# Kernel optimization log

Hardware: AMD Instinct MI355X
Metric: run time of the kernel (lower is better)

Reference implementation:

```python
import jax, jax.numpy as jnp
import numpy as np

N_NODES = 50000
N_EDGES = 500000
F_DIM = 128
N_REL = 8
N_LAYERS = 2
NEG_SLOPE = 0.2  # PyG RGATConv default negative_slope


def setup_inputs() -> dict:
    key = jax.random.key(0)
    ks = jax.random.split(key, 6)
    x = jax.random.normal(ks[0], (N_NODES, F_DIM), dtype=jnp.float32)
    edge_index = jax.random.randint(ks[1], (2, N_EDGES), 0, N_NODES)
    edge_type = jax.random.randint(ks[2], (N_EDGES,), 0, N_REL)
    # Per-layer relation weights [L, R, F_in, F_out], attention vectors q,k [L, F_out, 1], bias [L, F_out]
    W = jax.random.normal(ks[3], (N_LAYERS, N_REL, F_DIM, F_DIM), dtype=jnp.float32) * (1.0 / np.sqrt(F_DIM)).astype(np.float32)
    att_q = jax.random.normal(ks[4], (N_LAYERS, F_DIM, 1), dtype=jnp.float32) * 0.1
    att_k = jax.random.normal(ks[5], (N_LAYERS, F_DIM, 1), dtype=jnp.float32) * 0.1
    bias = jnp.zeros((N_LAYERS, F_DIM), dtype=jnp.float32)
    return {"x": x, "W": W, "att_q": att_q, "att_k": att_k, "bias": bias,
            "edge_index": edge_index, "edge_type": edge_type}


def _segment_softmax(logits, seg, num_segments):
    # Numerically stable softmax over edges grouped by destination node.
    m = jax.ops.segment_max(logits, seg, num_segments=num_segments)
    m = jax.lax.stop_gradient(m)
    e = jnp.exp(logits - m[seg])
    denom = jax.ops.segment_sum(e, seg, num_segments=num_segments)
    return e / (denom[seg] + 1e-16)


def _rgat_layer(h, src, dst, edge_type, W, q, k, b):
    # h: [N, F]; W: [R, F, F]. Project once per relation, then gather per edge
    # (avoids materializing [E, F, F] per-edge weight gathers).
    n = h.shape[0]
    xw = jnp.einsum('nf,rfg->rng', h, W)          # [R, N, F]
    out_j = xw[edge_type, src]                    # [E, F] transformed source feats
    out_i = xw[edge_type, dst]                    # [E, F] transformed dest feats
    # additive self-attention: leaky_relu(q(x_i) + k(x_j)), heads=1, dim=1
    logits = jax.nn.leaky_relu((out_i @ q + out_j @ k)[:, 0], NEG_SLOPE)  # [E]
    alpha = _segment_softmax(logits, dst, n)      # across-relation softmax per dst node
    agg = jax.ops.segment_sum(alpha[:, None] * out_j, dst, num_segments=n)  # [N, F]
    return agg + b


def reference(x, W, att_q, att_k, bias, edge_index, edge_type):
    src, dst = edge_index[0], edge_index[1]
    h = x
    for l in range(W.shape[0]):  # small fixed layer count
        h = _rgat_layer(h, src, dst, edge_type, W[l], att_q[l], att_k[l], bias[l])
        h = jax.nn.relu(h)  # dropout is identity in eval mode
    return h
```

## Files before the change

kernel.cpp:

```cpp
#include <hip/hip_runtime.h>
#include <hip/hip_bf16.h>
#include <hip/hip_fp16.h>

#define N_NODES 50000
#define N_EDGES 500000
#define F_DIM   128
#define N_REL   8
#define N_LAYERS 2
#define NEG_SLOPE 0.2f

#define NBLK_N ((N_NODES + 255) / 256)

typedef _Float16 half8 __attribute__((ext_vector_type(8)));
typedef float f32x4  __attribute__((ext_vector_type(4)));


__device__ inline float lrelu(float l) { return (l > 0.f) ? l : NEG_SLOPE * l; }

__global__ __launch_bounds__(256) void prep_h(const float* __restrict__ H,
                                              _Float16* __restrict__ Hf) {
    const size_t i8 = (size_t)blockIdx.x * 256 + threadIdx.x;
    if (i8 >= (size_t)N_NODES * F_DIM / 8) return;
    const float* src = H + i8 * 8;
    float av[8];
    *(float4*)(av)     = *(const float4*)(src);
    *(float4*)(av + 4) = *(const float4*)(src + 4);
    alignas(16) _Float16 hb[8];
#pragma unroll
    for (int j = 0; j < 8; ++j) hb[j] = (_Float16)av[j];
    *(uint4*)(Hf + i8 * 8) = *(const uint4*)hb;
}

__global__ __launch_bounds__(256) void prep_w(const float* __restrict__ W,
                                              _Float16* __restrict__ Wf) {
    __shared__ float tile[64][F_DIM + 1];
    const int mat = blockIdx.x;
    const float* src = W + (size_t)mat * F_DIM * F_DIM;
    const int t = threadIdx.x;
    for (int hf = 0; hf < 2; ++hf) {
#pragma unroll
        for (int i = 0; i < 8; ++i) {
            int idx = t + i * 256;
            int f = idx >> 5, c4 = idx & 31;
            float4 v = *(const float4*)(src + (size_t)(hf * 64 + f) * F_DIM + c4 * 4);
            *(float4*)&tile[f][c4 * 4] = v;
        }
        __syncthreads();
        int g = t >> 1, fs = (t & 1) * 32;
        for (int c = 0; c < 4; ++c) {
            alignas(16) _Float16 th[8];
#pragma unroll
            for (int j = 0; j < 8; ++j) th[j] = (_Float16)tile[fs + c * 8 + j][g];
            size_t o = ((size_t)mat * F_DIM + g) * F_DIM + hf * 64 + fs + c * 8;
            *(uint4*)(Wf + o) = *(const uint4*)th;
        }
        __syncthreads();
    }
}

#define GBM 128
#define RGRP 2
__global__ __launch_bounds__(256, 2) void gemm_xw(const _Float16* __restrict__ Hf,
                                                  const _Float16* __restrict__ Wf,
                                                  const float* __restrict__ qv_g,
                                                  const float* __restrict__ kv_g,
                                                  __half* __restrict__ xw,
                                                  float* __restrict__ a_q,
                                                  float* __restrict__ a_k) {
    __shared__ _Float16 lds[F_DIM * F_DIM];
    const int rb0 = blockIdx.x * GBM;
    const int r0  = blockIdx.y * RGRP;
    const int tid = threadIdx.x;
    const int lane = tid & 63, w = tid >> 6;
    const int q = lane >> 4, ln = lane & 15;

    half8 Af[2][4];
#pragma unroll
    for (int rt = 0; rt < 2; ++rt) {
        int row = rb0 + w * 32 + rt * 16 + ln;
        int ar = (row < N_NODES) ? row : (N_NODES - 1);
        const _Float16* hp = Hf + (size_t)ar * F_DIM;
#pragma unroll
        for (int ks = 0; ks < 4; ++ks)
            Af[rt][ks] = *(const half8*)(hp + ks * 32 + q * 8);
    }

    float qvl[8], kvl[8];
#pragma unroll
    for (int t = 0; t < 8; ++t) {
        qvl[t] = qv_g[t * 16 + ln];
        kvl[t] = kv_g[t * 16 + ln];
    }

    for (int rr = 0; rr < RGRP; ++rr) {
        const int r = r0 + rr;
        __syncthreads();
        {
            const _Float16* src = Wf + (size_t)r * F_DIM * F_DIM;
#pragma unroll
            for (int i = 0; i < 8; ++i) {
                int chunk = tid + i * 256;
                int gg = chunk >> 4, c8 = chunk & 15;
                uint4 v = *(const uint4*)(src + gg * F_DIM + c8 * 8);
                *(uint4*)(lds + gg * F_DIM + ((c8 ^ (gg & 15)) * 8)) = v;
            }
        }
        __syncthreads();

        f32x4 acc[2][8];
#pragma unroll
        for (int rt = 0; rt < 2; ++rt)
#pragma unroll
            for (int t = 0; t < 8; ++t) acc[rt][t] = (f32x4)(0.f);

#pragma unroll
        for (int ks = 0; ks < 4; ++ks) {
            const int jx = (((ks * 4 + q) ^ ln)) << 3;
            half8 Bf[8];
#pragma unroll
            for (int c = 0; c < 8; ++c)
                Bf[c] = *(const half8*)(lds + (c * 16 + ln) * F_DIM + jx);
#pragma unroll
            for (int c = 0; c < 8; ++c)
#pragma unroll
                for (int rt = 0; rt < 2; ++rt)
                    acc[rt][c] = __builtin_amdgcn_mfma_f32_16x16x32_f16(Af[rt][ks], Bf[c], acc[rt][c], 0, 0, 0);
        }

#pragma unroll
        for (int rt = 0; rt < 2; ++rt) {
            float pq[4], pk[4];
#pragma unroll
            for (int reg = 0; reg < 4; ++reg) {
                const int row = rb0 + w * 32 + rt * 16 + q * 4 + reg;
                alignas(16) unsigned short hs[8];
                float sq = 0.f, sk = 0.f;
#pragma unroll
                for (int t = 0; t < 8; ++t) {
                    float v = acc[rt][t][reg];
                    __half hv = __float2half(v);
                    hs[t] = *reinterpret_cast<unsigned short*>(&hv);
                    sq = fmaf(v, qvl[t], sq);
                    sk = fmaf(v, kvl[t], sk);
                }
                if (row < N_NODES)
                    *(uint4*)(xw + ((size_t)r * N_NODES + row) * F_DIM + ln * 8) = *(const uint4*)hs;
                pq[reg] = sq; pk[reg] = sk;
            }
#pragma unroll
            for (int reg = 0; reg < 4; ++reg) {
#pragma unroll
                for (int m = 1; m <= 8; m <<= 1) {
                    pq[reg] += __shfl_xor(pq[reg], m);
                    pk[reg] += __shfl_xor(pk[reg], m);
                }
            }
            if (ln == 0) {
#pragma unroll
                for (int reg = 0; reg < 4; ++reg) {
                    const int row = rb0 + w * 32 + rt * 16 + q * 4 + reg;
                    if (row < N_NODES) {
                        a_q[(size_t)row * N_REL + r] = pq[reg];
                        a_k[(size_t)row * N_REL + r] = pk[reg];
                    }
                }
            }
        }
    }
}


__global__ __launch_bounds__(256) void count_kernel(const int* __restrict__ dstp,
                                                    int* __restrict__ cnt) {
    int e = blockIdx.x * 256 + threadIdx.x;
    if (e < N_EDGES) atomicAdd(cnt + dstp[e], 1);
}

__global__ __launch_bounds__(256) void block_sum_kernel(const int* __restrict__ cnt,
                                                        int* __restrict__ partial) {
    __shared__ int s[256];
    int idx = blockIdx.x * 256 + threadIdx.x;
    int v = (idx < N_NODES) ? cnt[idx] : 0;
    s[threadIdx.x] = v;
    __syncthreads();
    for (int off = 128; off > 0; off >>= 1) {
        if (threadIdx.x < off) s[threadIdx.x] += s[threadIdx.x + off];
        __syncthreads();
    }
    if (threadIdx.x == 0) partial[blockIdx.x] = s[0];
}

__global__ __launch_bounds__(256) void scan_partials_kernel(int* __restrict__ partial,
                                                            int* __restrict__ row_ptr) {
    __shared__ int s[256];
    int t = threadIdx.x;
    int v = (t < NBLK_N) ? partial[t] : 0;
    s[t] = v;
    __syncthreads();
#pragma unroll
    for (int off = 1; off < 256; off <<= 1) {
        int x = (t >= off) ? s[t - off] : 0;
        __syncthreads();
        s[t] += x;
        __syncthreads();
    }
    if (t < NBLK_N) partial[t] = s[t] - v;
    if (t == 0) row_ptr[N_NODES] = N_EDGES;
}

__global__ __launch_bounds__(256) void scan_block_kernel(const int* __restrict__ cnt,
                                                         const int* __restrict__ partial,
                                                         int* __restrict__ row_ptr) {
    __shared__ int s[256];
    int t = threadIdx.x;
    int idx = blockIdx.x * 256 + t;
    int v = (idx < N_NODES) ? cnt[idx] : 0;
    s[t] = v;
    __syncthreads();
#pragma unroll
    for (int off = 1; off < 256; off <<= 1) {
        int x = (t >= off) ? s[t - off] : 0;
        __syncthreads();
        s[t] += x;
        __syncthreads();
    }
    if (idx < N_NODES) row_ptr[idx] = partial[blockIdx.x] + s[t] - v;
}

__global__ __launch_bounds__(256) void scatter_kernel(const int* __restrict__ srcp,
                                                      const int* __restrict__ dstp,
                                                      const int* __restrict__ etp,
                                                      const int* __restrict__ row_ptr,
                                                      int* __restrict__ cursor,
                                                      unsigned* __restrict__ sorted,
                                                      unsigned short* __restrict__ dst16) {
    int e = blockIdx.x * 256 + threadIdx.x;
    if (e >= N_EDGES) return;
    int d = dstp[e];
    int pos = atomicAdd(cursor + d, 1);
    int j = row_ptr[d] + pos;
    sorted[j] = (unsigned)srcp[e] | ((unsigned)etp[e] << 16);
    dst16[j] = (unsigned short)d;
}

__global__ __launch_bounds__(256) void logits_kernel(const float* __restrict__ a_q,
                                                     const float* __restrict__ a_k,
                                                     const unsigned* __restrict__ sorted,
                                                     const unsigned short* __restrict__ dst16,
                                                     float* __restrict__ lgt) {
    int j = blockIdx.x * 256 + threadIdx.x;
    if (j >= N_EDGES) return;
    unsigned p = sorted[j];
    int s = p & 0xffff, t = p >> 16;
    int d = dst16[j];
    lgt[j] = lrelu(a_q[(size_t)d * N_REL + t] + a_k[(size_t)s * N_REL + t]);
}

__device__ inline void accum8(float* acc, uint4 v, float a) {
    const __half2* h2 = reinterpret_cast<const __half2*>(&v);
#pragma unroll
    for (int t = 0; t < 4; ++t) {
        float2 f = __half22float2(h2[t]);
        acc[t * 2]     = fmaf(a, f.x, acc[t * 2]);
        acc[t * 2 + 1] = fmaf(a, f.y, acc[t * 2 + 1]);
    }
}
__device__ inline const uint4* xwrow(const __half* xw, unsigned p, int ln) {
    return (const uint4*)(xw + (((size_t)(p >> 16)) * N_NODES + (p & 0xffff)) * F_DIM + ln * 8);
}

__global__ __launch_bounds__(256) void agg_fused(const __half* __restrict__ xw,
                                                 const float* __restrict__ lgt,
                                                 const int* __restrict__ row_ptr,
                                                 const unsigned* __restrict__ sorted,
                                                 const float* __restrict__ bias,
                                                 float* __restrict__ outp,
                                                 _Float16* __restrict__ hfp) {
    const int lane = threadIdx.x & 63;
    const int wave = threadIdx.x >> 6;
    const int d = blockIdx.x * 4 + wave;
    if (d >= N_NODES) return;
    const int beg = row_ptr[d], end = row_ptr[d + 1];
    const int cnt = end - beg;
    const int g = lane >> 4, ln = lane & 15;

    if (cnt <= 64) {
        unsigned p = 0;
        float l = -3.4e38f;
        if (lane < cnt) {
            p = sorted[beg + lane];
            l = lgt[beg + lane];
        }
        float m = l;
#pragma unroll
        for (int off = 32; off > 0; off >>= 1) m = fmaxf(m, __shfl_xor(m, off));
        const float ex = (lane < cnt) ? __expf(l - m) : 0.f;

        float acc[8] = {0, 0, 0, 0, 0, 0, 0, 0};
        for (int i = 0; i < cnt; i += 16) {
            const bool b1 = (i + 4) < cnt, b2 = (i + 8) < cnt, b3 = (i + 12) < cnt;
            unsigned p0 = __shfl(p, i + g);
            float a0 = __shfl(ex, i + g);
            uint4 v0 = *xwrow(xw, p0, ln);
            uint4 v1, v2, v3;
            float a1 = 0.f, a2 = 0.f, a3 = 0.f;
            if (b1) { unsigned q1 = __shfl(p, i + 4 + g);  a1 = __shfl(ex, i + 4 + g);  v1 = *xwrow(xw, q1, ln); }
            if (b2) { unsigned q2 = __shfl(p, i + 8 + g);  a2 = __shfl(ex, i + 8 + g);  v2 = *xwrow(xw, q2, ln); }
            if (b3) { unsigned q3 = __shfl(p, i + 12 + g); a3 = __shfl(ex, i + 12 + g); v3 = *xwrow(xw, q3, ln); }
            accum8(acc, v0, a0);
            if (b1) accum8(acc, v1, a1);
            if (b2) accum8(acc, v2, a2);
            if (b3) accum8(acc, v3, a3);
        }
        float dsum = ex;
#pragma unroll
        for (int off = 32; off > 0; off >>= 1) dsum += __shfl_xor(dsum, off);
#pragma unroll
        for (int t = 0; t < 8; ++t) {
            acc[t] += __shfl_xor(acc[t], 16);
            acc[t] += __shfl_xor(acc[t], 32);
        }
        if (g == 0) {
            const float inv = 1.f / (dsum + 1e-16f);
#pragma unroll
            for (int t = 0; t < 8; ++t) {
                const int col = t * 16 + ln;
                const float v = fmaxf(fmaf(acc[t], inv, bias[col]), 0.f);
                if (outp) outp[(size_t)d * F_DIM + col] = v;
                if (hfp)  hfp[(size_t)d * F_DIM + col] = (_Float16)v;
            }
        }
    } else {
        const int p0 = lane * 2;
        const int c0 = (p0 & 7) * 16 + (p0 >> 3);
        const int c1 = c0 + 16;
        float2 acc = make_float2(bias[c0], bias[c1]);
        float m = -3.4e38f;
        for (int i = beg + lane; i < end; i += 64) m = fmaxf(m, lgt[i]);
#pragma unroll
        for (int off = 32; off > 0; off >>= 1) m = fmaxf(m, __shfl_xor(m, off));
        float dsum = 0.f;
        for (int i = beg + lane; i < end; i += 64) dsum += __expf(lgt[i] - m);
#pragma unroll
        for (int off = 32; off > 0; off >>= 1) dsum += __shfl_xor(dsum, off);
        const float inv = 1.f / (dsum + 1e-16f);
        for (int i = beg; i < end; ++i) {
            unsigned p = sorted[i];
            float alpha = __expf(lgt[i] - m) * inv;
            const __half2 h2 = *((const __half2*)xw + (((size_t)(p >> 16)) * N_NODES + (p & 0xffff)) * (F_DIM / 2) + lane);
            float2 v = make_float2(__half2float(h2.x), __half2float(h2.y));
            acc.x = fmaf(alpha, v.x, acc.x);
            acc.y = fmaf(alpha, v.y, acc.y);
        }
        const float v0 = fmaxf(acc.x, 0.f), v1 = fmaxf(acc.y, 0.f);
        if (outp) { outp[(size_t)d * F_DIM + c0] = v0; outp[(size_t)d * F_DIM + c1] = v1; }
        if (hfp)  { hfp[(size_t)d * F_DIM + c0] = (_Float16)v0; hfp[(size_t)d * F_DIM + c1] = (_Float16)v1; }
    }
}


extern "C" void kernel_launch(void* const* d_in, const int* in_sizes, int n_in,
                              void* d_out, int out_size, void* d_ws, size_t ws_size,
                              hipStream_t stream) {
    const float* x     = (const float*)d_in[0];
    const float* W     = (const float*)d_in[1];
    const float* att_q = (const float*)d_in[2];
    const float* att_k = (const float*)d_in[3];
    const float* bias  = (const float*)d_in[4];
    const int* ei      = (const int*)d_in[5];
    const int* etp     = (const int*)d_in[6];
    const int* srcp = ei;
    const int* dstp = ei + N_EDGES;
    float* out = (float*)d_out;
    char* ws   = (char*)d_ws;

    size_t off = 0;
    auto alloc = [&](size_t bytes) {
        void* p = ws + off;
        off = (off + bytes + 511) & ~(size_t)511;
        return p;
    };
    __half* xw       = (__half*)alloc((size_t)N_REL * N_NODES * F_DIM * sizeof(__half));
    float* a_q       = (float*)alloc((size_t)N_NODES * N_REL * sizeof(float));
    float* a_k       = (float*)alloc((size_t)N_NODES * N_REL * sizeof(float));
    int* cnt         = (int*)alloc((size_t)2 * N_NODES * sizeof(int));
    int* cursor      = cnt + N_NODES;
    int* row_ptr     = (int*)alloc(((size_t)N_NODES + 1) * sizeof(int));
    int* partial     = (int*)alloc(256 * sizeof(int));
    unsigned* sorted = (unsigned*)alloc((size_t)N_EDGES * sizeof(unsigned));
    unsigned short* dst16 = (unsigned short*)alloc((size_t)N_EDGES * sizeof(unsigned short));
    float* lgt       = (float*)alloc((size_t)N_EDGES * sizeof(float));
    _Float16* Wf     = (_Float16*)alloc((size_t)N_LAYERS * N_REL * F_DIM * F_DIM * sizeof(_Float16));
    _Float16* Hf     = (_Float16*)alloc((size_t)N_NODES * F_DIM * sizeof(_Float16));

    prep_w<<<N_LAYERS * N_REL, 256, 0, stream>>>(W, Wf);
    hipMemsetAsync(cnt, 0, (size_t)2 * N_NODES * 4, stream);
    count_kernel<<<(N_EDGES + 255) / 256, 256, 0, stream>>>(dstp, cnt);
    block_sum_kernel<<<NBLK_N, 256, 0, stream>>>(cnt, partial);
    scan_partials_kernel<<<1, 256, 0, stream>>>(partial, row_ptr);
    scan_block_kernel<<<NBLK_N, 256, 0, stream>>>(cnt, partial, row_ptr);
    scatter_kernel<<<(N_EDGES + 255) / 256, 256, 0, stream>>>(
        srcp, dstp, etp, row_ptr, cursor, sorted, dst16);

    const int grid_h = (N_NODES * F_DIM / 8 + 255) / 256;
    const int grid_m = (N_NODES + GBM - 1) / GBM;
    const int grid_e = (N_EDGES + 255) / 256;
    prep_h<<<grid_h, 256, 0, stream>>>(x, Hf);
    for (int l = 0; l < N_LAYERS; ++l) {
        gemm_xw<<<dim3(grid_m, N_REL / RGRP), 256, 0, stream>>>(
            Hf, Wf + (size_t)l * N_REL * F_DIM * F_DIM,
            att_q + l * F_DIM, att_k + l * F_DIM,
            xw, a_q, a_k);
        logits_kernel<<<grid_e, 256, 0, stream>>>(a_q, a_k, sorted, dst16, lgt);
        const bool last = (l == N_LAYERS - 1);
        agg_fused<<<(N_NODES + 3) / 4, 256, 0, stream>>>(
            xw, lgt, row_ptr, sorted, bias + l * F_DIM,
            last ? out : nullptr,
            last ? nullptr : Hf);
    }
}
```

Before: 311.3 us.

## Split GEMM to one relation per block, transpose attention scores, shorten aggregation unroll

The projection GEMM now launches one block per relation instead of two relations per block, which doubles the grid. Each block issues its weight-tile LDS load before its activation loads and needs only one barrier. The per-node attention scalars a_q/a_k move from [N,R] to [R,N] layout, so GEMM writes and logits gathers index by relation first. The aggregation loop now processes 8 edges per step with two unconditional gathers instead of 16 edges with guarded gathers. This removes branches but leaves fewer loads in flight, and it relies on out-of-range lanes holding safe indices and zero weights.

```diff
diff --git a/kernel.cpp b/kernel.cpp
--- a/kernel.cpp
+++ b/kernel.cpp
@@ -59,7 +59,6 @@
 }
 
 #define GBM 128
-#define RGRP 2
 __global__ __launch_bounds__(256, 2) void gemm_xw(const _Float16* __restrict__ Hf,
                                                   const _Float16* __restrict__ Wf,
                                                   const float* __restrict__ qv_g,
@@ -69,10 +68,21 @@
                                                   float* __restrict__ a_k) {
     __shared__ _Float16 lds[F_DIM * F_DIM];
     const int rb0 = blockIdx.x * GBM;
-    const int r0  = blockIdx.y * RGRP;
+    const int r   = blockIdx.y;
     const int tid = threadIdx.x;
     const int lane = tid & 63, w = tid >> 6;
     const int q = lane >> 4, ln = lane & 15;
+
+    {
+        const _Float16* src = Wf + (size_t)r * F_DIM * F_DIM;
+#pragma unroll
+        for (int i = 0; i < 8; ++i) {
+            int chunk = tid + i * 256;
+            int gg = chunk >> 4, c8 = chunk & 15;
+            uint4 v = *(const uint4*)(src + gg * F_DIM + c8 * 8);
+            *(uint4*)(lds + gg * F_DIM + ((c8 ^ (gg & 15)) * 8)) = v;
+        }
+    }
 
     half8 Af[2][4];
 #pragma unroll
@@ -92,77 +102,63 @@
         kvl[t] = kv_g[t * 16 + ln];
     }
 
-    for (int rr = 0; rr < RGRP; ++rr) {
-        const int r = r0 + rr;
-        __syncthreads();
-        {
-            const _Float16* src = Wf + (size_t)r * F_DIM * F_DIM;
-#pragma unroll
-            for (int i = 0; i < 8; ++i) {
-                int chunk = tid + i * 256;
-                int gg = chunk >> 4, c8 = chunk & 15;
-                uint4 v = *(const uint4*)(src + gg * F_DIM + c8 * 8);
-                *(uint4*)(lds + gg * F_DIM + ((c8 ^ (gg & 15)) * 8)) = v;
+    __syncthreads();
+
+    f32x4 acc[2][8];
+#pragma unroll
+    for (int rt = 0; rt < 2; ++rt)
+#pragma unroll
+        for (int t = 0; t < 8; ++t) acc[rt][t] = (f32x4)(0.f);
+
+#pragma unroll
+    for (int ks = 0; ks < 4; ++ks) {
+        const int jx = (((ks * 4 + q) ^ ln)) << 3;
+        half8 Bf[8];
+#pragma unroll
+        for (int c = 0; c < 8; ++c)
+            Bf[c] = *(const half8*)(lds + (c * 16 + ln) * F_DIM + jx);
+#pragma unroll
+        for (int c = 0; c < 8; ++c)
+#pragma unroll
+            for (int rt = 0; rt < 2; ++rt)
+                acc[rt][c] = __builtin_amdgcn_mfma_f32_16x16x32_f16(Af[rt][ks], Bf[c], acc[rt][c], 0, 0, 0);
+    }
+
+#pragma unroll
+    for (int rt = 0; rt < 2; ++rt) {
+        float pq[4], pk[4];
+#pragma unroll
+        for (int reg = 0; reg < 4; ++reg) {
+            const int row = rb0 + w * 32 + rt * 16 + q * 4 + reg;
+            alignas(16) unsigned short hs[8];
+            float sq = 0.f, sk = 0.f;
+#pragma unroll
+            for (int t = 0; t < 8; ++t) {
+                float v = acc[rt][t][reg];
+                __half hv = __float2half(v);
+                hs[t] = *reinterpret_cast<unsigned short*>(&hv);
+                sq = fmaf(v, qvl[t], sq);
+                sk = fmaf(v, kvl[t], sk);
             }
-        }
-        __syncthreads();
-
-        f32x4 acc[2][8];
-#pragma unroll
-        for (int rt = 0; rt < 2; ++rt)
-#pragma unroll
-            for (int t = 0; t < 8; ++t) acc[rt][t] = (f32x4)(0.f);
-
-#pragma unroll
-        for (int ks = 0; ks < 4; ++ks) {
-            const int jx = (((ks * 4 + q) ^ ln)) << 3;
-            half8 Bf[8];
-#pragma unroll
-            for (int c = 0; c < 8; ++c)
-                Bf[c] = *(const half8*)(lds + (c * 16 + ln) * F_DIM + jx);
-#pragma unroll
-            for (int c = 0; c < 8; ++c)
-#pragma unroll
-                for (int rt = 0; rt < 2; ++rt)
-                    acc[rt][c] = __builtin_amdgcn_mfma_f32_16x16x32_f16(Af[rt][ks], Bf[c], acc[rt][c], 0, 0, 0);
-        }
-
-#pragma unroll
-        for (int rt = 0; rt < 2; ++rt) {
-            float pq[4], pk[4];
+            if (row < N_NODES)
+                *(uint4*)(xw + ((size_t)r * N_NODES + row) * F_DIM + ln * 8) = *(const uint4*)hs;
+            pq[reg] = sq; pk[reg] = sk;
+        }
+#pragma unroll
+        for (int reg = 0; reg < 4; ++reg) {
+#pragma unroll
+            for (int m = 1; m <= 8; m <<= 1) {
+                pq[reg] += __shfl_xor(pq[reg], m);
+                pk[reg] += __shfl_xor(pk[reg], m);
+            }
+        }
+        if (ln == 0) {
 #pragma unroll
             for (int reg = 0; reg < 4; ++reg) {
                 const int row = rb0 + w * 32 + rt * 16 + q * 4 + reg;
-                alignas(16) unsigned short hs[8];
-                float sq = 0.f, sk = 0.f;
-#pragma unroll
-                for (int t = 0; t < 8; ++t) {
-                    float v = acc[rt][t][reg];
-                    __half hv = __float2half(v);
-                    hs[t] = *reinterpret_cast<unsigned short*>(&hv);
-                    sq = fmaf(v, qvl[t], sq);
-                    sk = fmaf(v, kvl[t], sk);
-                }
-                if (row < N_NODES)
-                    *(uint4*)(xw + ((size_t)r * N_NODES + row) * F_DIM + ln * 8) = *(const uint4*)hs;
-                pq[reg] = sq; pk[reg] = sk;
-            }
-#pragma unroll
-            for (int reg = 0; reg < 4; ++reg) {
-#pragma unroll
-                for (int m = 1; m <= 8; m <<= 1) {
-                    pq[reg] += __shfl_xor(pq[reg], m);
-                    pk[reg] += __shfl_xor(pk[reg], m);
-                }
-            }
-            if (ln == 0) {
-#pragma unroll
-                for (int reg = 0; reg < 4; ++reg) {
-                    const int row = rb0 + w * 32 + rt * 16 + q * 4 + reg;
-                    if (row < N_NODES) {
-                        a_q[(size_t)row * N_REL + r] = pq[reg];
-                        a_k[(size_t)row * N_REL + r] = pk[reg];
-                    }
+                if (row < N_NODES) {
+                    a_q[r * N_NODES + row] = pq[reg];
+                    a_k[r * N_NODES + row] = pk[reg];
                 }
             }
         }
@@ -253,7 +249,7 @@
     unsigned p = sorted[j];
     int s = p & 0xffff, t = p >> 16;
     int d = dst16[j];
-    lgt[j] = lrelu(a_q[(size_t)d * N_REL + t] + a_k[(size_t)s * N_REL + t]);
+    lgt[j] = lrelu(a_q[t * N_NODES + d] + a_k[t * N_NODES + s]);
 }
 
 __device__ inline void accum8(float* acc, uint4 v, float a) {
@@ -297,20 +293,15 @@
         const float ex = (lane < cnt) ? __expf(l - m) : 0.f;
 
         float acc[8] = {0, 0, 0, 0, 0, 0, 0, 0};
-        for (int i = 0; i < cnt; i += 16) {
-            const bool b1 = (i + 4) < cnt, b2 = (i + 8) < cnt, b3 = (i + 12) < cnt;
+        for (int i = 0; i < cnt; i += 8) {
             unsigned p0 = __shfl(p, i + g);
+            unsigned p1 = __shfl(p, i + 4 + g);
             float a0 = __shfl(ex, i + g);
+            float a1 = __shfl(ex, i + 4 + g);
             uint4 v0 = *xwrow(xw, p0, ln);
-            uint4 v1, v2, v3;
-            float a1 = 0.f, a2 = 0.f, a3 = 0.f;
-            if (b1) { unsigned q1 = __shfl(p, i + 4 + g);  a1 = __shfl(ex, i + 4 + g);  v1 = *xwrow(xw, q1, ln); }
-            if (b2) { unsigned q2 = __shfl(p, i + 8 + g);  a2 = __shfl(ex, i + 8 + g);  v2 = *xwrow(xw, q2, ln); }
-            if (b3) { unsigned q3 = __shfl(p, i + 12 + g); a3 = __shfl(ex, i + 12 + g); v3 = *xwrow(xw, q3, ln); }
+            uint4 v1 = *xwrow(xw, p1, ln);
             accum8(acc, v0, a0);
-            if (b1) accum8(acc, v1, a1);
-            if (b2) accum8(acc, v2, a2);
-            if (b3) accum8(acc, v3, a3);
+            accum8(acc, v1, a1);
         }
         float dsum = ex;
 #pragma unroll
@@ -381,8 +372,8 @@
         return p;
     };
     __half* xw       = (__half*)alloc((size_t)N_REL * N_NODES * F_DIM * sizeof(__half));
-    float* a_q       = (float*)alloc((size_t)N_NODES * N_REL * sizeof(float));
-    float* a_k       = (float*)alloc((size_t)N_NODES * N_REL * sizeof(float));
+    float* a_q       = (float*)alloc((size_t)N_REL * N_NODES * sizeof(float));
+    float* a_k       = (float*)alloc((size_t)N_REL * N_NODES * sizeof(float));
     int* cnt         = (int*)alloc((size_t)2 * N_NODES * sizeof(int));
     int* cursor      = cnt + N_NODES;
     int* row_ptr     = (int*)alloc(((size_t)N_NODES + 1) * sizeof(int));
@@ -407,7 +398,7 @@
     const int grid_e = (N_EDGES + 255) / 256;
     prep_h<<<grid_h, 256, 0, stream>>>(x, Hf);
     for (int l = 0; l < N_LAYERS; ++l) {
-        gemm_xw<<<dim3(grid_m, N_REL / RGRP), 256, 0, stream>>>(
+        gemm_xw<<<dim3(grid_m, N_REL), 256, 0, stream>>>(
             Hf, Wf + (size_t)l * N_REL * F_DIM * F_DIM,
             att_q + l * F_DIM, att_k + l * F_DIM,
             xw, a_q, a_k);
```

New measurement: 301.5 us. 1.03x faster.
